# Performance work log

Measured on AMD Instinct MI355X. Metric: run time of the kernel, lower is better.

## Reference

```python
import jax, jax.numpy as jnp
import numpy as np

B, N, D = 2, 2048, 512
H, HD = 8, 64
R = 64  # graph_radius
SCALE = HD ** -0.5
LN_EPS = 1e-5


def _ln(x, g, b):
    m = jnp.mean(x, axis=-1, keepdims=True)
    v = jnp.mean((x - m) ** 2, axis=-1, keepdims=True)
    return (x - m) * jax.lax.rsqrt(v + LN_EPS) * g + b


def setup_inputs() -> dict:
    key = jax.random.key(0)
    ks = jax.random.split(key, 8)
    w = lambda k, shape: (jax.random.normal(k, shape, jnp.float32) * 0.02)
    return {
        "nodes": jax.random.normal(ks[0], (B, N, D), jnp.float32),
        "ln1_g": jnp.ones((D,), jnp.float32), "ln1_b": jnp.zeros((D,), jnp.float32),
        "qkv_w": w(ks[1], (D, 3 * D)), "qkv_b": jnp.zeros((3 * D,), jnp.float32),
        "proj_w": w(ks[2], (D, D)), "proj_b": jnp.zeros((D,), jnp.float32),
        "rep_scale": jnp.ones((H,), jnp.float32),
        "rel_bias": w(ks[3], (2 * N - 1, H)),
        "ln2_g": jnp.ones((D,), jnp.float32), "ln2_b": jnp.zeros((D,), jnp.float32),
        "mlp_w1": w(ks[4], (D, 2 * D)), "mlp_b1": jnp.zeros((2 * D,), jnp.float32),
        "mlp_w2": w(ks[5], (2 * D, D)), "mlp_b2": jnp.zeros((D,), jnp.float32),
    }


def reference(nodes, ln1_g, ln1_b, qkv_w, qkv_b, proj_w, proj_b, rep_scale,
              rel_bias, ln2_g, ln2_b, mlp_w1, mlp_b1, mlp_w2, mlp_b2):
    b, n, d = nodes.shape
    x = _ln(nodes, ln1_g, ln1_b)                       # [B,N,D]
    qkv = (x @ qkv_w + qkv_b).reshape(b, n, 3, H, HD)
    qkv = jnp.transpose(qkv, (2, 0, 3, 1, 4))          # [3,B,H,N,HD]
    q, k, v = qkv[0], qkv[1], qkv[2]
    logits = jnp.einsum('bhnd,bhmd->bhnm', q, k) * SCALE
    # representation correlation (F.normalize with eps=1e-12)
    rep = x / jnp.maximum(jnp.linalg.norm(x, axis=-1, keepdims=True), 1e-12)
    corr = jnp.einsum('bnd,bmd->bnm', rep, rep)        # [B,N,N]
    logits = logits + corr[:, None] * rep_scale[None, :, None, None]
    pos = jnp.arange(n)
    relidx = pos[:, None] - pos[None, :]               # [N,N]
    bias = rel_bias[relidx + n - 1]                    # [N,N,H]
    logits = logits + jnp.transpose(bias, (2, 0, 1))[None]
    mask = jnp.abs(relidx) <= R
    logits = jnp.where(mask[None, None], logits, -jnp.inf)
    attn = jax.nn.softmax(logits, axis=-1)
    upd = jnp.einsum('bhnm,bhmd->bnhd', attn, v).reshape(b, n, d)
    nodes = nodes + (upd @ proj_w + proj_b)
    y = _ln(nodes, ln2_g, ln2_b)
    h = jax.nn.gelu(y @ mlp_w1 + mlp_b1, approximate=False)
    return nodes + (h @ mlp_w2 + mlp_b2)
```

## Files before the change

### kernel.cpp

```cpp
#include <hip/hip_runtime.h>
#include <math.h>

typedef __bf16 bf16;
typedef __bf16 bf16x4 __attribute__((ext_vector_type(4)));
typedef __bf16 bf16x8 __attribute__((ext_vector_type(8)));
typedef float floatx4 __attribute__((ext_vector_type(4)));

#define BB 2
#define NN 2048
#define DD 512
#define HH 8
#define HD 64
#define RR 64
#define D3 1536
#define NEG_BIG (-1e30f)
#define TQ 32
#define TBAND 160
#define VW 200

#define GL2LDS16(g, l)                                                        \
    __builtin_amdgcn_global_load_lds(                                         \
        (const __attribute__((address_space(1))) void*)(const void*)(g),      \
        (__attribute__((address_space(3))) void*)(void*)(l), 16, 0, 0)

__global__ __launch_bounds__(256) void cvt_t_kernel(
    const float* __restrict__ W, bf16* __restrict__ Wt, int K, int N) {
    __shared__ bf16 Ts[64][72];
    const int tid = threadIdx.x;
    const int n0 = blockIdx.x * 64, k0 = blockIdx.y * 64;
    #pragma unroll
    for (int i = 0; i < 4; i++) {
        int r = (tid >> 4) + i * 16;
        int c = (tid & 15) * 4;
        floatx4 v = *(const floatx4*)(W + (size_t)(k0 + r) * N + n0 + c);
        #pragma unroll
        for (int e = 0; e < 4; e++) Ts[r][c + e] = (bf16)v[e];
    }
    __syncthreads();
    #pragma unroll
    for (int i = 0; i < 4; i++) {
        int n = (tid >> 4) + i * 16;
        int k = (tid & 15) * 4;
        bf16x4 o;
        #pragma unroll
        for (int e = 0; e < 4; e++) o[e] = Ts[k + e][n];
        *(bf16x4*)(Wt + (size_t)(n0 + n) * K + k0 + k) = o;
    }
}

__device__ inline float block_reduce_sum256(float v, float* sbuf) {
    const int tid = threadIdx.x;
    #pragma unroll
    for (int o = 32; o > 0; o >>= 1) v += __shfl_xor(v, o, 64);
    __syncthreads();
    if ((tid & 63) == 0) sbuf[tid >> 6] = v;
    __syncthreads();
    return sbuf[0] + sbuf[1] + sbuf[2] + sbuf[3];
}

template <bool WANT_INV>
__global__ __launch_bounds__(256) void ln_kernel(
    const float* __restrict__ in, const float* __restrict__ gw,
    const float* __restrict__ bw, bf16* __restrict__ out,
    float* __restrict__ invnorm) {
    __shared__ float sbuf[4];
    const int row = blockIdx.x, tid = threadIdx.x;
    const int i0 = tid * 2;
    const float* ip = in + (size_t)row * DD;
    float v0 = ip[i0], v1 = ip[i0 + 1];
    float mean = block_reduce_sum256(v0 + v1, sbuf) * (1.f / DD);
    float d0 = v0 - mean, d1 = v1 - mean;
    float var = block_reduce_sum256(d0 * d0 + d1 * d1, sbuf) * (1.f / DD);
    float rs = rsqrtf(var + 1e-5f);
    float x0 = d0 * rs * gw[i0] + bw[i0];
    float x1 = d1 * rs * gw[i0 + 1] + bw[i0 + 1];
    out[(size_t)row * DD + i0] = (bf16)x0;
    out[(size_t)row * DD + i0 + 1] = (bf16)x1;
    if (WANT_INV) {
        float s2 = block_reduce_sum256(x0 * x0 + x1 * x1, sbuf);
        if (tid == 0) invnorm[row] = 1.f / fmaxf(sqrtf(s2), 1e-12f);
    }
}

template <int MODE>
__global__ __launch_bounds__(256) void gemm_bt(
    const bf16* __restrict__ A, const bf16* __restrict__ Bt,
    const float* __restrict__ bias, const float* __restrict__ resid,
    void* __restrict__ out, int M, int N, int K) {
    __shared__ __align__(16) bf16 As[2][64 * 64];
    __shared__ __align__(16) bf16 Bs[2][64 * 64];
    const int tid = threadIdx.x;
    const int w = tid >> 6, lane = tid & 63;
    const int lr = lane & 15, lq = lane >> 4;
    const int rowBase = blockIdx.y * 64, colBase = blockIdx.x * 64;
    const int wm = (w >> 1) * 32, wn = (w & 1) * 32;

    floatx4 acc[2][2];
    #pragma unroll
    for (int i = 0; i < 2; i++)
        #pragma unroll
        for (int j = 0; j < 2; j++) acc[i][j] = (floatx4){0.f, 0.f, 0.f, 0.f};

    auto stage = [&](int buf, int k0) {
        #pragma unroll
        for (int i = 0; i < 2; i++) {
            int g = i * 256 + tid;
            int row = g >> 3, k8 = (g & 7) ^ (row & 7);
            GL2LDS16(A + (size_t)(rowBase + row) * K + k0 + k8 * 8,
                     &As[buf][g * 8]);
        }
        #pragma unroll
        for (int i = 0; i < 2; i++) {
            int g = i * 256 + tid;
            int row = g >> 3, k8 = (g & 7) ^ (row & 7);
            GL2LDS16(Bt + (size_t)(colBase + row) * K + k0 + k8 * 8,
                     &Bs[buf][g * 8]);
        }
    };

    const int nsteps = K >> 6;
    stage(0, 0);
    for (int s = 0; s < nsteps; s++) {
        __syncthreads();
        if (s + 1 < nsteps) stage((s + 1) & 1, (s + 1) * 64);
        const int buf = s & 1;
        #pragma unroll
        for (int kb = 0; kb < 2; kb++) {
            bf16x8 af[2], bfr[2];
            #pragma unroll
            for (int i = 0; i < 2; i++) {
                int row = wm + i * 16 + lr;
                int g = row * 8 + ((kb * 4 + lq) ^ (row & 7));
                af[i] = *(bf16x8*)&As[buf][g * 8];
            }
            #pragma unroll
            for (int j = 0; j < 2; j++) {
                int row = wn + j * 16 + lr;
                int g = row * 8 + ((kb * 4 + lq) ^ (row & 7));
                bfr[j] = *(bf16x8*)&Bs[buf][g * 8];
            }
            #pragma unroll
            for (int i = 0; i < 2; i++)
                #pragma unroll
                for (int j = 0; j < 2; j++)
                    acc[i][j] = __builtin_amdgcn_mfma_f32_16x16x32_bf16(
                        af[i], bfr[j], acc[i][j], 0, 0, 0);
        }
    }

    #pragma unroll
    for (int i = 0; i < 2; i++) {
        #pragma unroll
        for (int j = 0; j < 2; j++) {
            #pragma unroll
            for (int r = 0; r < 4; r++) {
                int row = rowBase + wm + i * 16 + lq * 4 + r;
                int col = colBase + wn + j * 16 + lr;
                size_t idx = (size_t)row * N + col;
                float v = acc[i][j][r] + bias[col];
                if (MODE == 0) {
                    ((bf16*)out)[idx] = (bf16)v;
                } else if (MODE == 1) {
                    ((float*)out)[idx] = v + resid[idx];
                } else if (MODE == 2) {
                    float g = 0.5f * v * (1.f + erff(v * 0.70710678118654752f));
                    ((bf16*)out)[idx] = (bf16)g;
                } else {
                    ((float*)out)[idx] = v + resid[idx];
                }
            }
        }
    }
}

__global__ __launch_bounds__(256) void attn_kernel(
    const bf16* __restrict__ x, const float* __restrict__ invnorm,
    const bf16* __restrict__ qkv, const float* __restrict__ rep_scale,
    const float* __restrict__ rel_bias, bf16* __restrict__ upd) {
    __shared__ __align__(16) bf16 Qs[TQ][72];
    __shared__ __align__(16) bf16 Ks[TBAND][72];
    __shared__ __align__(16) bf16 Vt[64 * VW];
    __shared__ __align__(16) bf16 Ps[TQ][168];
    __shared__ float relb[4][192];
    __shared__ float invb[TBAND];
    __shared__ float rmax2[TQ][2];
    __shared__ float rsum2[TQ][2];

    const int tid = threadIdx.x;
    const int bid = blockIdx.x;
    const int b = bid & 1;
    const int h0 = ((bid >> 1) & 1) * 4;
    const int n0 = (bid >> 2) * TQ;
    const int bN = b * NN;

    const int w = tid >> 6, lane = tid & 63;
    const int lr = lane & 15, lq = lane >> 4;
    const int rowHalf = (w >> 1) * 16;
    const int colBase = (w & 1) * 80;
    const int c2 = (w & 1) * 32;

    if (tid < TBAND) {
        int mc = min(max(n0 - RR + tid, 0), NN - 1);
        invb[tid] = invnorm[bN + mc];
    }
    for (int idx = tid; idx < 4 * 191; idx += 256) {
        int hh = idx / 191, dh = idx - hh * 191;
        relb[hh][dh] = rel_bias[(size_t)(dh + (NN - 1 - 95)) * HH + h0 + hh];
    }

    floatx4 cacc[5];
    #pragma unroll
    for (int t = 0; t < 5; t++) cacc[t] = (floatx4){0.f, 0.f, 0.f, 0.f};

    for (int c = 0; c < 8; c++) {
        __syncthreads();
        #pragma unroll
        for (int i = 0; i < 5; i++) {
            int s = i * 256 + tid;
            int j = s >> 3, seg = s & 7;
            int mc = min(max(n0 - RR + j, 0), NN - 1);
            *(bf16x8*)&Ks[j][seg * 8] =
                *(const bf16x8*)(x + (size_t)(bN + mc) * DD + c * 64 + seg * 8);
        }
        __syncthreads();
        #pragma unroll
        for (int kb = 0; kb < 2; kb++) {
            bf16x8 a = *(bf16x8*)&Ks[64 + rowHalf + lr][kb * 32 + lq * 8];
            #pragma unroll
            for (int t = 0; t < 5; t++) {
                bf16x8 bb = *(bf16x8*)&Ks[colBase + t * 16 + lr][kb * 32 + lq * 8];
                cacc[t] = __builtin_amdgcn_mfma_f32_16x16x32_bf16(a, bb, cacc[t], 0, 0, 0);
            }
        }
    }
    __syncthreads();

    float corrv[5][4];
    {
        float invq[4];
        #pragma unroll
        for (int r = 0; r < 4; r++) invq[r] = invb[64 + rowHalf + lq * 4 + r];
        #pragma unroll
        for (int t = 0; t < 5; t++) {
            float invk = invb[colBase + t * 16 + lr];
            #pragma unroll
            for (int r = 0; r < 4; r++) corrv[t][r] = cacc[t][r] * invq[r] * invk;
        }
    }

    for (int h = h0; h < h0 + 4; h++) {
        {
            int row = tid >> 3, seg = tid & 7;
            *(bf16x8*)&Qs[row][seg * 8] =
                *(const bf16x8*)(qkv + (size_t)(bN + n0 + row) * D3 + h * HD + seg * 8);
        }
        #pragma unroll
        for (int i = 0; i < 5; i++) {
            int s = i * 256 + tid;
            int j = s >> 3, seg = s & 7;
            int mc = min(max(n0 - RR + j, 0), NN - 1);
            *(bf16x8*)&Ks[j][seg * 8] =
                *(const bf16x8*)(qkv + (size_t)(bN + mc) * D3 + DD + h * HD + seg * 8);
            bf16x8 v = *(const bf16x8*)(qkv + (size_t)(bN + mc) * D3 + 2 * DD + h * HD + seg * 8);
            #pragma unroll
            for (int e = 0; e < 8; e++) {
                int d = seg * 8 + e;
                int key = (d >> 2) & 7;
                int jsw = (j & 7) | (((j >> 3) ^ key) << 3);
                Vt[d * VW + jsw] = v[e];
            }
        }
        __syncthreads();

        floatx4 sacc[5];
        #pragma unroll
        for (int t = 0; t < 5; t++) sacc[t] = (floatx4){0.f, 0.f, 0.f, 0.f};
        #pragma unroll
        for (int kb = 0; kb < 2; kb++) {
            bf16x8 a = *(bf16x8*)&Qs[rowHalf + lr][kb * 32 + lq * 8];
            #pragma unroll
            for (int t = 0; t < 5; t++) {
                bf16x8 bb = *(bf16x8*)&Ks[colBase + t * 16 + lr][kb * 32 + lq * 8];
                sacc[t] = __builtin_amdgcn_mfma_f32_16x16x32_bf16(a, bb, sacc[t], 0, 0, 0);
            }
        }

        const float srep = rep_scale[h];
        float l[5][4];
        float mx[4] = {NEG_BIG, NEG_BIG, NEG_BIG, NEG_BIG};
        #pragma unroll
        for (int t = 0; t < 5; t++) {
            int j = colBase + t * 16 + lr;
            int m = n0 - RR + j;
            #pragma unroll
            for (int r = 0; r < 4; r++) {
                int qi = rowHalf + lq * 4 + r;
                int relidx = qi + RR - j;
                bool valid = (relidx >= -RR) && (relidx <= RR) && (m >= 0) && (m < NN);
                float lv = sacc[t][r] * 0.125f + corrv[t][r] * srep +
                           relb[h - h0][relidx + 95];
                l[t][r] = valid ? lv : NEG_BIG;
                mx[r] = fmaxf(mx[r], l[t][r]);
            }
        }
        #pragma unroll
        for (int r = 0; r < 4; r++)
            #pragma unroll
            for (int mk = 1; mk <= 8; mk <<= 1)
                mx[r] = fmaxf(mx[r], __shfl_xor(mx[r], mk, 64));
        if (lr == 0) {
            #pragma unroll
            for (int r = 0; r < 4; r++) rmax2[rowHalf + lq * 4 + r][w & 1] = mx[r];
        }
        __syncthreads();

        float rm[4], sm[4];
        #pragma unroll
        for (int r = 0; r < 4; r++) {
            int row = rowHalf + lq * 4 + r;
            rm[r] = fmaxf(rmax2[row][0], rmax2[row][1]);
            sm[r] = 0.f;
        }
        #pragma unroll
        for (int t = 0; t < 5; t++) {
            int j = colBase + t * 16 + lr;
            #pragma unroll
            for (int r = 0; r < 4; r++) {
                float pv = __expf(l[t][r] - rm[r]);
                sm[r] += pv;
                Ps[rowHalf + lq * 4 + r][j] = (bf16)pv;
            }
        }
        #pragma unroll
        for (int r = 0; r < 4; r++)
            #pragma unroll
            for (int mk = 1; mk <= 8; mk <<= 1)
                sm[r] += __shfl_xor(sm[r], mk, 64);
        if (lr == 0) {
            #pragma unroll
            for (int r = 0; r < 4; r++) rsum2[rowHalf + lq * 4 + r][w & 1] = sm[r];
        }
        __syncthreads();

        floatx4 oacc[2] = {(floatx4){0.f, 0.f, 0.f, 0.f}, (floatx4){0.f, 0.f, 0.f, 0.f}};
        #pragma unroll
        for (int kb = 0; kb < 5; kb++) {
            bf16x8 a = *(bf16x8*)&Ps[rowHalf + lr][kb * 32 + lq * 8];
            #pragma unroll
            for (int tt = 0; tt < 2; tt++) {
                int d = c2 + tt * 16 + lr;
                int key = (d >> 2) & 7;
                int jsw = (kb * 32 + lq * 8) ^ (key << 3);
                bf16x8 bb = *(bf16x8*)&Vt[d * VW + jsw];
                oacc[tt] = __builtin_amdgcn_mfma_f32_16x16x32_bf16(a, bb, oacc[tt], 0, 0, 0);
            }
        }
        #pragma unroll
        for (int r = 0; r < 4; r++) {
            int row = rowHalf + lq * 4 + r;
            float rinv = 1.f / (rsum2[row][0] + rsum2[row][1]);
            #pragma unroll
            for (int tt = 0; tt < 2; tt++) {
                upd[(size_t)(bN + n0 + row) * DD + h * HD + c2 + tt * 16 + lr] =
                    (bf16)(oacc[tt][r] * rinv);
            }
        }
        __syncthreads();
    }
}

extern "C" void kernel_launch(void* const* d_in, const int* in_sizes, int n_in,
                              void* d_out, int out_size, void* d_ws,
                              size_t ws_size, hipStream_t stream) {
    const float* nodes  = (const float*)d_in[0];
    const float* ln1_g  = (const float*)d_in[1];
    const float* ln1_b  = (const float*)d_in[2];
    const float* qkv_w  = (const float*)d_in[3];
    const float* qkv_b  = (const float*)d_in[4];
    const float* proj_w = (const float*)d_in[5];
    const float* proj_b = (const float*)d_in[6];
    const float* rep_s  = (const float*)d_in[7];
    const float* rel_b  = (const float*)d_in[8];
    const float* ln2_g  = (const float*)d_in[9];
    const float* ln2_b  = (const float*)d_in[10];
    const float* mlp_w1 = (const float*)d_in[11];
    const float* mlp_b1 = (const float*)d_in[12];
    const float* mlp_w2 = (const float*)d_in[13];
    const float* mlp_b2 = (const float*)d_in[14];

    char* p = (char*)d_ws;
    float* invn = (float*)p;            p += (size_t)1 << 20;
    bf16*  wqt  = (bf16*)p;             p += (size_t)DD * D3 * 2;
    bf16*  wpt  = (bf16*)p;             p += (size_t)DD * DD * 2;
    bf16*  w1t  = (bf16*)p;             p += (size_t)DD * 2 * DD * 2;
    bf16*  w2t  = (bf16*)p;             p += (size_t)2 * DD * DD * 2;
    bf16*  x    = (bf16*)p;             p += (size_t)BB * NN * DD * 2;
    bf16*  qkvb = (bf16*)p;             p += (size_t)BB * NN * D3 * 2;
    float* mid  = (float*)p;            p += (size_t)BB * NN * DD * 4;
    bf16*  y    = x;
    bf16*  hgl  = qkvb;
    bf16*  upd  = (bf16*)d_out;

    const int M = BB * NN;

    cvt_t_kernel<<<dim3(D3 / 64, DD / 64), 256, 0, stream>>>(qkv_w, wqt, DD, D3);
    cvt_t_kernel<<<dim3(DD / 64, DD / 64), 256, 0, stream>>>(proj_w, wpt, DD, DD);
    cvt_t_kernel<<<dim3(2 * DD / 64, DD / 64), 256, 0, stream>>>(mlp_w1, w1t, DD, 2 * DD);
    cvt_t_kernel<<<dim3(DD / 64, 2 * DD / 64), 256, 0, stream>>>(mlp_w2, w2t, 2 * DD, DD);

    ln_kernel<true><<<M, 256, 0, stream>>>(nodes, ln1_g, ln1_b, x, invn);
    gemm_bt<0><<<dim3(D3 / 64, M / 64), 256, 0, stream>>>(
        x, wqt, qkv_b, nullptr, qkvb, M, D3, DD);
    attn_kernel<<<(NN / TQ) * 2 * BB, 256, 0, stream>>>(
        x, invn, qkvb, rep_s, rel_b, upd);
    gemm_bt<1><<<dim3(DD / 64, M / 64), 256, 0, stream>>>(
        upd, wpt, proj_b, nodes, mid, M, DD, DD);
    ln_kernel<false><<<M, 256, 0, stream>>>(mid, ln2_g, ln2_b, y, nullptr);
    gemm_bt<2><<<dim3(2 * DD / 64, M / 64), 256, 0, stream>>>(
        y, w1t, mlp_b1, nullptr, hgl, M, 2 * DD, DD);
    gemm_bt<3><<<dim3(DD / 64, M / 64), 256, 0, stream>>>(
        hgl, w2t, mlp_b2, mid, (float*)d_out, M, DD, 2 * DD);
}
```

Before: 182.8 us.

## Split corr and V-transpose into separate kernels, use direct LDS loads in attention

Moves the band correlation GEMM out of the attention kernel into its own kernel, which writes normalized corr tiles to workspace. This removes the correlation work that was repeated for each of the two head-group blocks. A separate kernel pre-transposes V to a head-major layout, so the attention kernel can fill Q, K and V^T tiles with global_load_lds instead of register round-trips and scalar LDS scatter. The four weight-conversion launches are also merged into one. The cost is extra launches, a global round-trip for corr and Vt that aliases the mid buffer, and a changed LDS layout that drops the old swizzle and the trailing barrier.

```diff
diff --git a/kernel.cpp b/kernel.cpp
--- a/kernel.cpp
+++ b/kernel.cpp
@@ -16,18 +16,26 @@
 #define NEG_BIG (-1e30f)
 #define TQ 32
 #define TBAND 160
-#define VW 200
 
 #define GL2LDS16(g, l)                                                        \
     __builtin_amdgcn_global_load_lds(                                         \
         (const __attribute__((address_space(1))) void*)(const void*)(g),      \
         (__attribute__((address_space(3))) void*)(void*)(l), 16, 0, 0)
 
-__global__ __launch_bounds__(256) void cvt_t_kernel(
-    const float* __restrict__ W, bf16* __restrict__ Wt, int K, int N) {
+__global__ __launch_bounds__(256) void cvt_all_kernel(
+    const float* __restrict__ qkv_w, const float* __restrict__ proj_w,
+    const float* __restrict__ m1w, const float* __restrict__ m2w,
+    bf16* __restrict__ wqt, bf16* __restrict__ wpt,
+    bf16* __restrict__ w1t, bf16* __restrict__ w2t) {
     __shared__ bf16 Ts[64][72];
     const int tid = threadIdx.x;
-    const int n0 = blockIdx.x * 64, k0 = blockIdx.y * 64;
+    int bid = blockIdx.x;
+    const float* W; bf16* Wt; int K, N, bx, by;
+    if (bid < 192)      { W = qkv_w;  Wt = wqt; K = 512;  N = 1536; bx = bid % 24; by = bid / 24; }
+    else if (bid < 256) { bid -= 192; W = proj_w; Wt = wpt; K = 512;  N = 512;  bx = bid % 8;  by = bid / 8; }
+    else if (bid < 384) { bid -= 256; W = m1w;  Wt = w1t; K = 512;  N = 1024; bx = bid % 16; by = bid / 16; }
+    else                { bid -= 384; W = m2w;  Wt = w2t; K = 1024; N = 512;  bx = bid % 8;  by = bid / 8; }
+    const int n0 = bx * 64, k0 = by * 64;
     #pragma unroll
     for (int i = 0; i < 4; i++) {
         int r = (tid >> 4) + i * 16;
@@ -106,15 +114,13 @@
         for (int i = 0; i < 2; i++) {
             int g = i * 256 + tid;
             int row = g >> 3, k8 = (g & 7) ^ (row & 7);
-            GL2LDS16(A + (size_t)(rowBase + row) * K + k0 + k8 * 8,
-                     &As[buf][g * 8]);
+            GL2LDS16(A + (size_t)(rowBase + row) * K + k0 + k8 * 8, &As[buf][g * 8]);
         }
         #pragma unroll
         for (int i = 0; i < 2; i++) {
             int g = i * 256 + tid;
             int row = g >> 3, k8 = (g & 7) ^ (row & 7);
-            GL2LDS16(Bt + (size_t)(colBase + row) * K + k0 + k8 * 8,
-                     &Bs[buf][g * 8]);
+            GL2LDS16(Bt + (size_t)(colBase + row) * K + k0 + k8 * 8, &Bs[buf][g * 8]);
         }
     };
 
@@ -173,16 +179,97 @@
     }
 }
 
+__global__ __launch_bounds__(256) void corr_kernel(
+    const bf16* __restrict__ x, const float* __restrict__ invnorm,
+    float* __restrict__ corr_g) {
+    __shared__ __align__(16) bf16 Xc[TBAND * 72];
+    __shared__ float invb[TBAND];
+    const int tid = threadIdx.x;
+    const int b = blockIdx.x & 1, n0 = (blockIdx.x >> 1) * TQ;
+    const int bN = b * NN;
+    const int w = tid >> 6, lane = tid & 63;
+    const int lr = lane & 15, lq = lane >> 4;
+    const int rowHalf = (w >> 1) * 16, colBase = (w & 1) * 80;
+
+    if (tid < TBAND) {
+        int mc = min(max(n0 - RR + tid, 0), NN - 1);
+        invb[tid] = invnorm[bN + mc];
+    }
+
+    floatx4 cacc[5];
+    #pragma unroll
+    for (int t = 0; t < 5; t++) cacc[t] = (floatx4){0.f, 0.f, 0.f, 0.f};
+
+    for (int c = 0; c < 8; c++) {
+        __syncthreads();
+        #pragma unroll
+        for (int rr = 0; rr < 6; rr++) {
+            int G = rr * 256 + tid;
+            if (G < 1440) {
+                int j = G / 9, gc = G % 9;
+                int gcs = min(gc, 7);
+                int mc = min(max(n0 - RR + j, 0), NN - 1);
+                GL2LDS16(x + (size_t)(bN + mc) * DD + c * 64 + gcs * 8, Xc + G * 8);
+            }
+        }
+        __syncthreads();
+        #pragma unroll
+        for (int kb = 0; kb < 2; kb++) {
+            bf16x8 a = *(bf16x8*)&Xc[(64 + rowHalf + lr) * 72 + kb * 32 + lq * 8];
+            #pragma unroll
+            for (int t = 0; t < 5; t++) {
+                bf16x8 bb = *(bf16x8*)&Xc[(colBase + t * 16 + lr) * 72 + kb * 32 + lq * 8];
+                cacc[t] = __builtin_amdgcn_mfma_f32_16x16x32_bf16(a, bb, cacc[t], 0, 0, 0);
+            }
+        }
+    }
+
+    float invq[4];
+    #pragma unroll
+    for (int r = 0; r < 4; r++) invq[r] = invb[64 + rowHalf + lq * 4 + r];
+    const size_t cbase = (size_t)blockIdx.x * TQ * TBAND;
+    #pragma unroll
+    for (int t = 0; t < 5; t++) {
+        float invk = invb[colBase + t * 16 + lr];
+        #pragma unroll
+        for (int r = 0; r < 4; r++)
+            corr_g[cbase + (size_t)(rowHalf + lq * 4 + r) * TBAND + colBase + t * 16 + lr] =
+                cacc[t][r] * invq[r] * invk;
+    }
+}
+
+__global__ __launch_bounds__(256) void vtrans_kernel(
+    const bf16* __restrict__ qkvb, bf16* __restrict__ vt_g) {
+    __shared__ bf16 Ts[64][72];
+    const int tid = threadIdx.x;
+    const int r0 = blockIdx.x * 64;
+    const int h = blockIdx.y;
+    #pragma unroll
+    for (int i = 0; i < 2; i++) {
+        int r = (tid >> 3) + i * 32, c8 = tid & 7;
+        *(bf16x8*)&Ts[r][c8 * 8] =
+            *(const bf16x8*)(qkvb + (size_t)(r0 + r) * D3 + 2 * DD + h * HD + c8 * 8);
+    }
+    __syncthreads();
+    #pragma unroll
+    for (int i = 0; i < 2; i++) {
+        int d = (tid >> 3) + i * 32, c8 = (tid & 7) * 8;
+        bf16x8 o;
+        #pragma unroll
+        for (int e = 0; e < 8; e++) o[e] = Ts[c8 + e][d];
+        *(bf16x8*)(vt_g + (((size_t)(h * HD + d)) << 12) + r0 + c8) = o;
+    }
+}
+
 __global__ __launch_bounds__(256) void attn_kernel(
-    const bf16* __restrict__ x, const float* __restrict__ invnorm,
-    const bf16* __restrict__ qkv, const float* __restrict__ rep_scale,
+    const bf16* __restrict__ qkv, const bf16* __restrict__ vt_g,
+    const float* __restrict__ corr_g, const float* __restrict__ rep_scale,
     const float* __restrict__ rel_bias, bf16* __restrict__ upd) {
-    __shared__ __align__(16) bf16 Qs[TQ][72];
-    __shared__ __align__(16) bf16 Ks[TBAND][72];
-    __shared__ __align__(16) bf16 Vt[64 * VW];
-    __shared__ __align__(16) bf16 Ps[TQ][168];
+    __shared__ __align__(16) bf16 Qs[TQ * 264];
+    __shared__ __align__(16) bf16 Ks[TBAND * 72];
+    __shared__ __align__(16) bf16 Vt[64 * 168];
+    __shared__ __align__(16) bf16 Ps[TQ * 168];
     __shared__ float relb[4][192];
-    __shared__ float invb[TBAND];
     __shared__ float rmax2[TQ][2];
     __shared__ float rsum2[TQ][2];
 
@@ -192,82 +279,57 @@
     const int h0 = ((bid >> 1) & 1) * 4;
     const int n0 = (bid >> 2) * TQ;
     const int bN = b * NN;
-
     const int w = tid >> 6, lane = tid & 63;
     const int lr = lane & 15, lq = lane >> 4;
     const int rowHalf = (w >> 1) * 16;
     const int colBase = (w & 1) * 80;
     const int c2 = (w & 1) * 32;
 
-    if (tid < TBAND) {
-        int mc = min(max(n0 - RR + tid, 0), NN - 1);
-        invb[tid] = invnorm[bN + mc];
-    }
     for (int idx = tid; idx < 4 * 191; idx += 256) {
         int hh = idx / 191, dh = idx - hh * 191;
         relb[hh][dh] = rel_bias[(size_t)(dh + (NN - 1 - 95)) * HH + h0 + hh];
     }
 
-    floatx4 cacc[5];
-    #pragma unroll
-    for (int t = 0; t < 5; t++) cacc[t] = (floatx4){0.f, 0.f, 0.f, 0.f};
-
-    for (int c = 0; c < 8; c++) {
-        __syncthreads();
-        #pragma unroll
-        for (int i = 0; i < 5; i++) {
-            int s = i * 256 + tid;
-            int j = s >> 3, seg = s & 7;
-            int mc = min(max(n0 - RR + j, 0), NN - 1);
-            *(bf16x8*)&Ks[j][seg * 8] =
-                *(const bf16x8*)(x + (size_t)(bN + mc) * DD + c * 64 + seg * 8);
-        }
-        __syncthreads();
-        #pragma unroll
-        for (int kb = 0; kb < 2; kb++) {
-            bf16x8 a = *(bf16x8*)&Ks[64 + rowHalf + lr][kb * 32 + lq * 8];
-            #pragma unroll
-            for (int t = 0; t < 5; t++) {
-                bf16x8 bb = *(bf16x8*)&Ks[colBase + t * 16 + lr][kb * 32 + lq * 8];
-                cacc[t] = __builtin_amdgcn_mfma_f32_16x16x32_bf16(a, bb, cacc[t], 0, 0, 0);
-            }
-        }
-    }
-    __syncthreads();
-
     float corrv[5][4];
     {
-        float invq[4];
-        #pragma unroll
-        for (int r = 0; r < 4; r++) invq[r] = invb[64 + rowHalf + lq * 4 + r];
-        #pragma unroll
-        for (int t = 0; t < 5; t++) {
-            float invk = invb[colBase + t * 16 + lr];
-            #pragma unroll
-            for (int r = 0; r < 4; r++) corrv[t][r] = cacc[t][r] * invq[r] * invk;
+        const size_t cbase = (size_t)(((bid >> 2) << 1) | b) * TQ * TBAND;
+        #pragma unroll
+        for (int t = 0; t < 5; t++)
+            #pragma unroll
+            for (int r = 0; r < 4; r++)
+                corrv[t][r] = corr_g[cbase + (size_t)(rowHalf + lq * 4 + r) * TBAND +
+                                     colBase + t * 16 + lr];
+    }
+
+    #pragma unroll
+    for (int rr = 0; rr < 5; rr++) {
+        int G = rr * 256 + tid;
+        if (G < 1056) {
+            int q = G / 33, gc = G % 33;
+            int gcs = min(gc, 31);
+            GL2LDS16(qkv + (size_t)(bN + n0 + q) * D3 + h0 * HD + gcs * 8, Qs + G * 8);
         }
     }
 
     for (int h = h0; h < h0 + 4; h++) {
-        {
-            int row = tid >> 3, seg = tid & 7;
-            *(bf16x8*)&Qs[row][seg * 8] =
-                *(const bf16x8*)(qkv + (size_t)(bN + n0 + row) * D3 + h * HD + seg * 8);
-        }
-        #pragma unroll
-        for (int i = 0; i < 5; i++) {
-            int s = i * 256 + tid;
-            int j = s >> 3, seg = s & 7;
-            int mc = min(max(n0 - RR + j, 0), NN - 1);
-            *(bf16x8*)&Ks[j][seg * 8] =
-                *(const bf16x8*)(qkv + (size_t)(bN + mc) * D3 + DD + h * HD + seg * 8);
-            bf16x8 v = *(const bf16x8*)(qkv + (size_t)(bN + mc) * D3 + 2 * DD + h * HD + seg * 8);
-            #pragma unroll
-            for (int e = 0; e < 8; e++) {
-                int d = seg * 8 + e;
-                int key = (d >> 2) & 7;
-                int jsw = (j & 7) | (((j >> 3) ^ key) << 3);
-                Vt[d * VW + jsw] = v[e];
+        __syncthreads();
+        #pragma unroll
+        for (int rr = 0; rr < 6; rr++) {
+            int G = rr * 256 + tid;
+            if (G < 1440) {
+                int j = G / 9, gc = G % 9;
+                int gcs = min(gc, 7);
+                int mc = min(max(n0 - RR + j, 0), NN - 1);
+                GL2LDS16(qkv + (size_t)(bN + mc) * D3 + DD + h * HD + gcs * 8, Ks + G * 8);
+            }
+        }
+        #pragma unroll
+        for (int rr = 0; rr < 6; rr++) {
+            int G = rr * 256 + tid;
+            if (G < 1344) {
+                int d = G / 21, gc = G % 21;
+                int nsrc = min(max(n0 - RR + gc * 8, 0), NN - 8);
+                GL2LDS16(vt_g + (((size_t)(h * HD + d)) << 12) + bN + nsrc, Vt + G * 8);
             }
         }
         __syncthreads();
@@ -277,10 +339,10 @@
         for (int t = 0; t < 5; t++) sacc[t] = (floatx4){0.f, 0.f, 0.f, 0.f};
         #pragma unroll
         for (int kb = 0; kb < 2; kb++) {
-            bf16x8 a = *(bf16x8*)&Qs[rowHalf + lr][kb * 32 + lq * 8];
+            bf16x8 a = *(bf16x8*)&Qs[(rowHalf + lr) * 264 + (h - h0) * 64 + kb * 32 + lq * 8];
             #pragma unroll
             for (int t = 0; t < 5; t++) {
-                bf16x8 bb = *(bf16x8*)&Ks[colBase + t * 16 + lr][kb * 32 + lq * 8];
+                bf16x8 bb = *(bf16x8*)&Ks[(colBase + t * 16 + lr) * 72 + kb * 32 + lq * 8];
                 sacc[t] = __builtin_amdgcn_mfma_f32_16x16x32_bf16(a, bb, sacc[t], 0, 0, 0);
             }
         }
@@ -328,7 +390,7 @@
             for (int r = 0; r < 4; r++) {
                 float pv = __expf(l[t][r] - rm[r]);
                 sm[r] += pv;
-                Ps[rowHalf + lq * 4 + r][j] = (bf16)pv;
+                Ps[(rowHalf + lq * 4 + r) * 168 + j] = (bf16)pv;
             }
         }
         #pragma unroll
@@ -345,13 +407,10 @@
         floatx4 oacc[2] = {(floatx4){0.f, 0.f, 0.f, 0.f}, (floatx4){0.f, 0.f, 0.f, 0.f}};
         #pragma unroll
         for (int kb = 0; kb < 5; kb++) {
-            bf16x8 a = *(bf16x8*)&Ps[rowHalf + lr][kb * 32 + lq * 8];
+            bf16x8 a = *(bf16x8*)&Ps[(rowHalf + lr) * 168 + kb * 32 + lq * 8];
             #pragma unroll
             for (int tt = 0; tt < 2; tt++) {
-                int d = c2 + tt * 16 + lr;
-                int key = (d >> 2) & 7;
-                int jsw = (kb * 32 + lq * 8) ^ (key << 3);
-                bf16x8 bb = *(bf16x8*)&Vt[d * VW + jsw];
+                bf16x8 bb = *(bf16x8*)&Vt[(c2 + tt * 16 + lr) * 168 + kb * 32 + lq * 8];
                 oacc[tt] = __builtin_amdgcn_mfma_f32_16x16x32_bf16(a, bb, oacc[tt], 0, 0, 0);
             }
         }
@@ -365,7 +424,6 @@
                     (bf16)(oacc[tt][r] * rinv);
             }
         }
-        __syncthreads();
     }
 }
 
@@ -396,23 +454,25 @@
     bf16*  w2t  = (bf16*)p;             p += (size_t)2 * DD * DD * 2;
     bf16*  x    = (bf16*)p;             p += (size_t)BB * NN * DD * 2;
     bf16*  qkvb = (bf16*)p;             p += (size_t)BB * NN * D3 * 2;
-    float* mid  = (float*)p;            p += (size_t)BB * NN * DD * 4;
+    char*  regA = p;                    p += (size_t)BB * NN * DD * 4;
+    float* corr_g = (float*)regA;
+    bf16*  vt_g   = (bf16*)(regA + (size_t)BB * (NN / TQ) * TQ * TBAND * 4);
+    float* mid    = (float*)regA;
     bf16*  y    = x;
     bf16*  hgl  = qkvb;
     bf16*  upd  = (bf16*)d_out;
 
     const int M = BB * NN;
 
-    cvt_t_kernel<<<dim3(D3 / 64, DD / 64), 256, 0, stream>>>(qkv_w, wqt, DD, D3);
-    cvt_t_kernel<<<dim3(DD / 64, DD / 64), 256, 0, stream>>>(proj_w, wpt, DD, DD);
-    cvt_t_kernel<<<dim3(2 * DD / 64, DD / 64), 256, 0, stream>>>(mlp_w1, w1t, DD, 2 * DD);
-    cvt_t_kernel<<<dim3(DD / 64, 2 * DD / 64), 256, 0, stream>>>(mlp_w2, w2t, 2 * DD, DD);
-
+    cvt_all_kernel<<<512, 256, 0, stream>>>(qkv_w, proj_w, mlp_w1, mlp_w2,
+                                            wqt, wpt, w1t, w2t);
     ln_kernel<true><<<M, 256, 0, stream>>>(nodes, ln1_g, ln1_b, x, invn);
+    corr_kernel<<<BB * (NN / TQ), 256, 0, stream>>>(x, invn, corr_g);
     gemm_bt<0><<<dim3(D3 / 64, M / 64), 256, 0, stream>>>(
         x, wqt, qkv_b, nullptr, qkvb, M, D3, DD);
+    vtrans_kernel<<<dim3(M / 64, HH), 256, 0, stream>>>(qkvb, vt_g);
     attn_kernel<<<(NN / TQ) * 2 * BB, 256, 0, stream>>>(
-        x, invn, qkvb, rep_s, rel_b, upd);
+        qkvb, vt_g, corr_g, rep_s, rel_b, upd);
     gemm_bt<1><<<dim3(DD / 64, M / 64), 256, 0, stream>>>(
         upd, wpt, proj_b, nodes, mid, M, DD, DD);
     ln_kernel<false><<<M, 256, 0, stream>>>(mid, ln2_g, ln2_b, y, nullptr);
```

Measured after the change: 179.2 us. -2.0%, faster.
